# Kernel optimization log

Measured on AMD Instinct MI355X. Metric: run time of the kernel, lower is better.

## Reference

```python
import jax, jax.numpy as jnp
import numpy as np

B, N, D4 = 32768, 20, 64  # embed_dim = 4 * D4 = 256
BIG = 1e10


def setup_inputs() -> dict:
    key = jax.random.key(0)
    ks = jax.random.split(key, 10)
    points = jax.random.normal(ks[0], (B, N, 3), dtype=jnp.float32)
    mask = (jax.random.uniform(ks[1], (B, N)) < 0.85).astype(jnp.float32)
    s = 0.1
    return {
        "points": points,
        "mask": mask,
        "W_rel": jax.random.normal(ks[2], (3, D4), jnp.float32) * s,
        "b_rel": jax.random.normal(ks[3], (D4,), jnp.float32) * s,
        "W_dist": jax.random.normal(ks[4], (1, D4), jnp.float32) * s,
        "b_dist": jax.random.normal(ks[5], (D4,), jnp.float32) * s,
        "emb_count": jax.random.normal(ks[6], (50, D4), jnp.float32) * s,
        "W_den": jax.random.normal(ks[7], (1, D4), jnp.float32) * s,
        "b_den": jax.random.normal(ks[8], (D4,), jnp.float32) * s,
    }


def _local_density(points, mask):
    # Batched replacement of the per-sample cdist+topk Python loop.
    b, n, _ = points.shape
    diff = points[:, :, None, :] - points[:, None, :, :]        # [B,N,N,3]
    d2 = jnp.sum(diff * diff, axis=-1)                          # [B,N,N]
    eye = jnp.eye(n, dtype=bool)
    pair_valid = (mask[:, :, None] > 0) & (mask[:, None, :] > 0) & ~eye
    d = jnp.where(pair_valid, jnp.sqrt(jnp.maximum(d2, 1e-12)), BIG)
    nearest = -jax.lax.top_k(-d, 3)[0]                          # 3 smallest dists, ascending
    nv = jnp.sum(mask, axis=1).astype(jnp.int32)                # [B] valid counts
    k = jnp.clip(jnp.minimum(3, nv - 1), 1, None)               # k = min(3, n_valid-1)
    w = (jnp.arange(3)[None, :] < k[:, None]).astype(points.dtype)  # [B,3]
    dens = jnp.sum(nearest * w[:, None, :], axis=-1) / k[:, None].astype(points.dtype)
    valid_row = (mask > 0) & (nv[:, None] > 1)                  # zero for invalid / n_valid<=1
    return jnp.where(valid_row, dens, 0.0)[..., None]           # [B,N,1]


def reference(points, mask, W_rel, b_rel, W_dist, b_dist, emb_count, W_den, b_den):
    b, n, _ = points.shape
    n_valid = jnp.clip(jnp.sum(mask, axis=1, keepdims=True), 1, None)    # [B,1]
    centroid = jnp.sum(points * mask[..., None], axis=1, keepdims=True) / n_valid[..., None]
    rel = points - centroid                                              # [B,N,3]
    rel_f = rel @ W_rel + b_rel                                          # [B,N,D4]
    cdist_ = jnp.linalg.norm(rel, axis=-1, keepdims=True)                # [B,N,1]
    dist_f = cdist_ @ W_dist + b_dist                                    # [B,N,D4]
    idx = n_valid[:, 0].astype(jnp.int32)                                # [B]
    count_f = jnp.broadcast_to(emb_count[idx][:, None, :], (b, n, emb_count.shape[1]))
    density = _local_density(points, mask)                               # [B,N,1]
    den_f = density @ W_den + b_den                                      # [B,N,D4]
    return jnp.concatenate([rel_f, dist_f, count_f, den_f], axis=-1)     # [B,N,4*D4]
```

## Files before the change

kernel.cpp:

```cpp
#include <hip/hip_runtime.h>
#include <math.h>

#define BIGD 1e10f
#define NPTS 20
#define BPB  4

typedef float f4 __attribute__((ext_vector_type(4)));

__global__ __launch_bounds__(256) void spf_kernel(
    const float* __restrict__ points,
    const float* __restrict__ mask,
    const float* __restrict__ W_rel,
    const float* __restrict__ b_rel,
    const float* __restrict__ W_dist,
    const float* __restrict__ b_dist,
    const float* __restrict__ emb_count,
    const float* __restrict__ W_den,
    const float* __restrict__ b_den,
    float* __restrict__ out,
    int B)
{
    const int w    = threadIdx.x >> 6;
    const int lane = threadIdx.x & 63;
    const int b    = blockIdx.x * BPB + w;
    const bool active = (b < B);

    __shared__ __align__(16) float sP[BPB][NPTS * 3];
    __shared__ __align__(16) float sM[BPB][NPTS];
    __shared__ float sDen[BPB][NPTS];
    __shared__ float sCd[BPB][NPTS];

    if (active) {
        if (lane < 15) {
            ((f4*)sP[w])[lane] = ((const f4*)points)[(size_t)b * 15 + lane];
        } else if (lane < 20) {
            ((f4*)sM[w])[lane - 15] = ((const f4*)mask)[(size_t)b * 5 + (lane - 15)];
        }
    }
    __syncthreads();

    float sm = 0.f, cx = 0.f, cy = 0.f, cz = 0.f;
#pragma unroll
    for (int i = 0; i < NPTS; ++i) {
        const float m = sM[w][i];
        sm += m;
        cx = fmaf(m, sP[w][i * 3 + 0], cx);
        cy = fmaf(m, sP[w][i * 3 + 1], cy);
        cz = fmaf(m, sP[w][i * 3 + 2], cz);
    }
    const float nvf = fmaxf(sm, 1.0f);
    cx /= nvf; cy /= nvf; cz /= nvf;
    const int nv  = (int)(sm + 0.5f);
    const int idx = (int)(nvf + 0.5f);

    if (active && lane < NPTS) {
        const int i = lane;
        const float mi = sM[w][i];
        const float px = sP[w][i * 3 + 0], py = sP[w][i * 3 + 1], pz = sP[w][i * 3 + 2];
        float b0 = BIGD, b1 = BIGD, b2 = BIGD;
#pragma unroll
        for (int j = 0; j < NPTS; ++j) {
            const float dx = px - sP[w][j * 3 + 0];
            const float dy = py - sP[w][j * 3 + 1];
            const float dz = pz - sP[w][j * 3 + 2];
            const float d2 = dx * dx + dy * dy + dz * dz;
            float d = sqrtf(fmaxf(d2, 1e-12f));
            const bool valid = (j != i) && (mi > 0.f) && (sM[w][j] > 0.f);
            d = valid ? d : BIGD;
            if (d < b0)      { b2 = b1; b1 = b0; b0 = d; }
            else if (d < b1) { b2 = b1; b1 = d; }
            else if (d < b2) { b2 = d; }
        }
        int k = min(3, nv - 1);
        k = max(k, 1);
        float s = b0;
        if (k > 1) s += b1;
        if (k > 2) s += b2;
        const float dens = s / (float)k;
        sDen[w][i] = ((mi > 0.f) && (nv > 1)) ? dens : 0.f;

        const float rx = px - cx, ry = py - cy, rz = pz - cz;
        sCd[w][i] = sqrtf(rx * rx + ry * ry + rz * rz);
    }
    __syncthreads();

    const int g      = lane;
    const int region = g >> 4;
    const int cq     = g & 15;

    f4 w0 = {0,0,0,0}, w1 = {0,0,0,0}, w2 = {0,0,0,0};
    f4 wd = {0,0,0,0}, bb = {0,0,0,0};
    if (region == 0) {
        w0 = ((const f4*)(W_rel +   0))[cq];
        w1 = ((const f4*)(W_rel +  64))[cq];
        w2 = ((const f4*)(W_rel + 128))[cq];
        bb = ((const f4*)b_rel)[cq];
    } else if (region == 1) {
        wd = ((const f4*)W_dist)[cq];
        bb = ((const f4*)b_dist)[cq];
    } else if (region == 2) {
        bb = ((const f4*)(emb_count + (size_t)idx * 64))[cq];
    } else {
        wd = ((const f4*)W_den)[cq];
        bb = ((const f4*)b_den)[cq];
    }
    const bool use_cd = (region == 1);

    if (active) {
        f4* __restrict__ outv = (f4*)(out + (size_t)b * (NPTS * 256));
#pragma unroll
        for (int n = 0; n < NPTS; ++n) {
            const float rx = sP[w][n * 3 + 0] - cx;
            const float ry = sP[w][n * 3 + 1] - cy;
            const float rz = sP[w][n * 3 + 2] - cz;
            const float sc = use_cd ? sCd[w][n] : sDen[w][n];
            f4 v;
            v.x = fmaf(rx, w0.x, fmaf(ry, w1.x, fmaf(rz, w2.x, fmaf(sc, wd.x, bb.x))));
            v.y = fmaf(rx, w0.y, fmaf(ry, w1.y, fmaf(rz, w2.y, fmaf(sc, wd.y, bb.y))));
            v.z = fmaf(rx, w0.z, fmaf(ry, w1.z, fmaf(rz, w2.z, fmaf(sc, wd.z, bb.z))));
            v.w = fmaf(rx, w0.w, fmaf(ry, w1.w, fmaf(rz, w2.w, fmaf(sc, wd.w, bb.w))));
            __builtin_nontemporal_store(v, &outv[n * 64 + g]);
        }
    }
}

extern "C" void kernel_launch(void* const* d_in, const int* in_sizes, int n_in,
                              void* d_out, int out_size, void* d_ws, size_t ws_size,
                              hipStream_t stream) {
    const float* points    = (const float*)d_in[0];
    const float* mask      = (const float*)d_in[1];
    const float* W_rel     = (const float*)d_in[2];
    const float* b_rel     = (const float*)d_in[3];
    const float* W_dist    = (const float*)d_in[4];
    const float* b_dist    = (const float*)d_in[5];
    const float* emb_count = (const float*)d_in[6];
    const float* W_den     = (const float*)d_in[7];
    const float* b_den     = (const float*)d_in[8];
    float* out             = (float*)d_out;

    const int B    = in_sizes[0] / (NPTS * 3);
    const int grid = (B + BPB - 1) / BPB;
    spf_kernel<<<grid, 256, 0, stream>>>(points, mask, W_rel, b_rel, W_dist, b_dist,
                                         emb_count, W_den, b_den, out, B);
}
```

Baseline: 680.8 us.

## Replace block barriers with wave-local LDS fences and pack point data into float4

Each wave handles its own batch element, so the block-wide __syncthreads is replaced by a per-wave s_waitcnt fence, and inactive waves return early. Points and mask are packed into one float4 per point in LDS, and relative coords plus centroid distance are precomputed into a second float4 array, cutting scalar LDS reads in the inner loops. The output store also switches from nontemporal to a regular store, which may change cache behaviour on this write-bound kernel. Relying on wave-synchronous LDS visibility without a barrier is a correctness assumption tied to the 64-lane wave.

```diff
diff --git a/kernel.cpp b/kernel.cpp
--- a/kernel.cpp
+++ b/kernel.cpp
@@ -6,6 +6,11 @@
 #define BPB  4
 
 typedef float f4 __attribute__((ext_vector_type(4)));
+
+__device__ __forceinline__ void wave_lds_fence() {
+    asm volatile("s_waitcnt lgkmcnt(0)" ::: "memory");
+    __builtin_amdgcn_sched_barrier(0);
+}
 
 __global__ __launch_bounds__(256) void spf_kernel(
     const float* __restrict__ points,
@@ -23,49 +28,48 @@
     const int w    = threadIdx.x >> 6;
     const int lane = threadIdx.x & 63;
     const int b    = blockIdx.x * BPB + w;
-    const bool active = (b < B);
+    if (b >= B) return;
 
-    __shared__ __align__(16) float sP[BPB][NPTS * 3];
-    __shared__ __align__(16) float sM[BPB][NPTS];
-    __shared__ float sDen[BPB][NPTS];
-    __shared__ float sCd[BPB][NPTS];
+    __shared__ __align__(16) f4    sPM[BPB][NPTS];
+    __shared__ __align__(16) f4    sRC[BPB][NPTS];
+    __shared__          float sDen[BPB][NPTS];
 
-    if (active) {
-        if (lane < 15) {
-            ((f4*)sP[w])[lane] = ((const f4*)points)[(size_t)b * 15 + lane];
-        } else if (lane < 20) {
-            ((f4*)sM[w])[lane - 15] = ((const f4*)mask)[(size_t)b * 5 + (lane - 15)];
-        }
+    if (lane < NPTS) {
+        const float* pp = points + (size_t)b * (NPTS * 3) + lane * 3;
+        f4 q;
+        q.x = pp[0]; q.y = pp[1]; q.z = pp[2];
+        q.w = mask[(size_t)b * NPTS + lane];
+        sPM[w][lane] = q;
     }
-    __syncthreads();
+    wave_lds_fence();
 
     float sm = 0.f, cx = 0.f, cy = 0.f, cz = 0.f;
 #pragma unroll
     for (int i = 0; i < NPTS; ++i) {
-        const float m = sM[w][i];
-        sm += m;
-        cx = fmaf(m, sP[w][i * 3 + 0], cx);
-        cy = fmaf(m, sP[w][i * 3 + 1], cy);
-        cz = fmaf(m, sP[w][i * 3 + 2], cz);
+        const f4 q = sPM[w][i];
+        sm += q.w;
+        cx = fmaf(q.w, q.x, cx);
+        cy = fmaf(q.w, q.y, cy);
+        cz = fmaf(q.w, q.z, cz);
     }
     const float nvf = fmaxf(sm, 1.0f);
     cx /= nvf; cy /= nvf; cz /= nvf;
     const int nv  = (int)(sm + 0.5f);
     const int idx = (int)(nvf + 0.5f);
 
-    if (active && lane < NPTS) {
-        const int i = lane;
-        const float mi = sM[w][i];
-        const float px = sP[w][i * 3 + 0], py = sP[w][i * 3 + 1], pz = sP[w][i * 3 + 2];
+    if (lane < NPTS) {
+        const f4 me = sPM[w][lane];
+        const float mi = me.w;
         float b0 = BIGD, b1 = BIGD, b2 = BIGD;
 #pragma unroll
         for (int j = 0; j < NPTS; ++j) {
-            const float dx = px - sP[w][j * 3 + 0];
-            const float dy = py - sP[w][j * 3 + 1];
-            const float dz = pz - sP[w][j * 3 + 2];
+            const f4 qj = sPM[w][j];
+            const float dx = me.x - qj.x;
+            const float dy = me.y - qj.y;
+            const float dz = me.z - qj.z;
             const float d2 = dx * dx + dy * dy + dz * dz;
             float d = sqrtf(fmaxf(d2, 1e-12f));
-            const bool valid = (j != i) && (mi > 0.f) && (sM[w][j] > 0.f);
+            const bool valid = (j != lane) && (mi > 0.f) && (qj.w > 0.f);
             d = valid ? d : BIGD;
             if (d < b0)      { b2 = b1; b1 = b0; b0 = d; }
             else if (d < b1) { b2 = b1; b1 = d; }
@@ -77,16 +81,17 @@
         if (k > 1) s += b1;
         if (k > 2) s += b2;
         const float dens = s / (float)k;
-        sDen[w][i] = ((mi > 0.f) && (nv > 1)) ? dens : 0.f;
+        sDen[w][lane] = ((mi > 0.f) && (nv > 1)) ? dens : 0.f;
 
-        const float rx = px - cx, ry = py - cy, rz = pz - cz;
-        sCd[w][i] = sqrtf(rx * rx + ry * ry + rz * rz);
+        f4 rc;
+        rc.x = me.x - cx; rc.y = me.y - cy; rc.z = me.z - cz;
+        rc.w = sqrtf(rc.x * rc.x + rc.y * rc.y + rc.z * rc.z);
+        sRC[w][lane] = rc;
     }
-    __syncthreads();
+    wave_lds_fence();
 
-    const int g      = lane;
-    const int region = g >> 4;
-    const int cq     = g & 15;
+    const int region = lane >> 4;
+    const int cq     = lane & 15;
 
     f4 w0 = {0,0,0,0}, w1 = {0,0,0,0}, w2 = {0,0,0,0};
     f4 wd = {0,0,0,0}, bb = {0,0,0,0};
@@ -106,21 +111,18 @@
     }
     const bool use_cd = (region == 1);
 
-    if (active) {
-        f4* __restrict__ outv = (f4*)(out + (size_t)b * (NPTS * 256));
+    f4* __restrict__ outv = (f4*)(out + (size_t)b * (NPTS * 256));
 #pragma unroll
-        for (int n = 0; n < NPTS; ++n) {
-            const float rx = sP[w][n * 3 + 0] - cx;
-            const float ry = sP[w][n * 3 + 1] - cy;
-            const float rz = sP[w][n * 3 + 2] - cz;
-            const float sc = use_cd ? sCd[w][n] : sDen[w][n];
-            f4 v;
-            v.x = fmaf(rx, w0.x, fmaf(ry, w1.x, fmaf(rz, w2.x, fmaf(sc, wd.x, bb.x))));
-            v.y = fmaf(rx, w0.y, fmaf(ry, w1.y, fmaf(rz, w2.y, fmaf(sc, wd.y, bb.y))));
-            v.z = fmaf(rx, w0.z, fmaf(ry, w1.z, fmaf(rz, w2.z, fmaf(sc, wd.z, bb.z))));
-            v.w = fmaf(rx, w0.w, fmaf(ry, w1.w, fmaf(rz, w2.w, fmaf(sc, wd.w, bb.w))));
-            __builtin_nontemporal_store(v, &outv[n * 64 + g]);
-        }
+    for (int n = 0; n < NPTS; ++n) {
+        const f4 rc = sRC[w][n];
+        const float dn = sDen[w][n];
+        const float sc = use_cd ? rc.w : dn;
+        f4 v;
+        v.x = fmaf(rc.x, w0.x, fmaf(rc.y, w1.x, fmaf(rc.z, w2.x, fmaf(sc, wd.x, bb.x))));
+        v.y = fmaf(rc.x, w0.y, fmaf(rc.y, w1.y, fmaf(rc.z, w2.y, fmaf(sc, wd.y, bb.y))));
+        v.z = fmaf(rc.x, w0.z, fmaf(rc.y, w1.z, fmaf(rc.z, w2.z, fmaf(sc, wd.z, bb.z))));
+        v.w = fmaf(rc.x, w0.w, fmaf(rc.y, w1.w, fmaf(rc.z, w2.w, fmaf(sc, wd.w, bb.w))));
+        outv[n * 64 + lane] = v;
     }
 }
 
```

Result: no change. 683.8 us (+0.4%).
